# Optimization experiments

Hardware: AMD Instinct MI355X
Metric: run time of the kernel (lower is better)

## Reference

```python
import jax, jax.numpy as jnp
import numpy as np

NUM_HEADS = 8
NUM_LEVEL = 4
KERNEL = 2
NUM_POINT = KERNEL * KERNEL
D_MODEL = 256
HEAD_DIM = D_MODEL // NUM_HEADS
REF_SIZE = 4
EPS = 1e-6


def _kernel_indices():
    # even kernel: linspace(-k/2+0.5, k/2-0.5, k) -> [-0.5, 0.5] for k=2
    ind = np.linspace(-KERNEL // 2 + 0.5, KERNEL // 2 - 0.5, KERNEL)
    i, j = np.meshgrid(ind, ind, indexing='ij')
    ki = np.stack([j, i], axis=-1).reshape(-1, 2) / KERNEL  # (P, 2), (x, y)
    return jnp.asarray(ki, dtype=jnp.float32)


def _ref_windows(shapes):
    # mask is None -> centers on a regular grid, size = ref_size / (H, W)
    refs = []
    for (H, W) in shapes:
        y = (jnp.arange(1, H + 1, dtype=jnp.float32) - 0.5) / (H + EPS)
        x = (jnp.arange(1, W + 1, dtype=jnp.float32) - 0.5) / (W + EPS)
        yy, xx = jnp.meshgrid(y, x, indexing='ij')           # (H, W)
        center = jnp.stack([xx, yy], axis=-1).reshape(-1, 2)  # (HW, 2)
        size = jnp.broadcast_to(
            jnp.array([REF_SIZE / W, REF_SIZE / H], dtype=jnp.float32), center.shape)
        refs.append(jnp.concatenate([center, size], axis=-1))
    return jnp.concatenate(refs, axis=0)  # (L, 4)


def _bilinear_sample(vflat, grid, H, W):
    """vflat: (B, H*W, M, D) one level; grid: (B, Lq, M, P, 2) normalized [0,1].
    Returns (B, Lq, M, P, D). Zero padding outside, align_corners=False."""
    B, _, M, D = vflat.shape
    x = grid[..., 0] * W - 0.5
    y = grid[..., 1] * H - 0.5
    x0 = jnp.floor(x); y0 = jnp.floor(y)
    lx = x - x0; ly = y - y0
    x0i = x0.astype(jnp.int32); y0i = y0.astype(jnp.int32)
    bidx = jnp.arange(B)[:, None, None, None]
    midx = jnp.arange(M)[None, None, :, None]

    def corner(xi, yi, w):
        valid = (xi >= 0) & (xi < W) & (yi >= 0) & (yi < H)
        idx = jnp.clip(yi, 0, H - 1) * W + jnp.clip(xi, 0, W - 1)
        g = vflat[bidx, idx, midx]  # (B, Lq, M, P, D)
        return g * (w * valid.astype(w.dtype))[..., None]

    out = corner(x0i, y0i, (1 - lx) * (1 - ly))
    out = out + corner(x0i + 1, y0i, lx * (1 - ly))
    out = out + corner(x0i, y0i + 1, (1 - lx) * ly)
    out = out + corner(x0i + 1, y0i + 1, lx * ly)
    return out


def setup_inputs() -> dict:
    key = jax.random.key(0)
    ks = jax.random.split(key, 20)
    spatial = [(100, 100), (50, 50), (25, 25), (13, 13)]
    B = 4
    inp = {}
    for i, (H, W) in enumerate(spatial):
        inp[f'value{i}'] = jax.random.normal(ks[i], (B, D_MODEL, H, W), dtype=jnp.float32)
        inp[f'pos{i}'] = jax.random.normal(ks[4 + i], (B, D_MODEL, H, W), dtype=jnp.float32)
    s = 0.05
    inp['Wv'] = jax.random.normal(ks[8], (D_MODEL, D_MODEL), dtype=jnp.float32) * s
    inp['bv'] = jnp.zeros((D_MODEL,), dtype=jnp.float32)
    inp['Wo'] = jax.random.normal(ks[9], (D_MODEL, D_MODEL), dtype=jnp.float32) * s
    inp['bo'] = jnp.zeros((D_MODEL,), dtype=jnp.float32)
    nb = NUM_LEVEL * NUM_HEADS * 4
    inp['Wbox'] = jax.random.normal(ks[10], (nb, D_MODEL), dtype=jnp.float32) * s
    inp['bbox'] = jax.random.uniform(ks[11], (nb,), dtype=jnp.float32)
    na = NUM_HEADS * NUM_LEVEL * NUM_POINT
    inp['Wattn'] = jax.random.normal(ks[12], (na, D_MODEL), dtype=jnp.float32) * s
    inp['battn'] = jax.random.normal(ks[13], (na,), dtype=jnp.float32) * s
    return inp


def reference(value0, value1, value2, value3, pos0, pos1, pos2, pos3,
              Wv, bv, Wo, bo, Wbox, bbox, Wattn, battn):
    levels = [value0, value1, value2, value3]
    poss = [pos0, pos1, pos2, pos3]
    shapes = [(v.shape[2], v.shape[3]) for v in levels]
    B = levels[0].shape[0]

    # flatten pyramid: (B, C, H, W) -> (B, HW, C)
    value = jnp.concatenate(
        [v.reshape(B, D_MODEL, -1).transpose(0, 2, 1) for v in levels], axis=1)
    pos = jnp.concatenate(
        [p.reshape(B, D_MODEL, -1).transpose(0, 2, 1) for p in poss], axis=1)
    L = value.shape[1]

    query = value + pos
    vp = (value @ Wv.T + bv).reshape(B, L, NUM_HEADS, HEAD_DIM)

    attn = jax.nn.softmax(
        (query @ Wattn.T + battn).reshape(B, L, NUM_HEADS, NUM_LEVEL * NUM_POINT),
        axis=-1).reshape(B, L, NUM_HEADS, NUM_LEVEL, NUM_POINT)

    offset = (query @ Wbox.T + bbox).reshape(B, L, NUM_HEADS, NUM_LEVEL, 4)
    ref = _ref_windows(shapes)[None, :, None, None, :]          # (1, L, 1, 1, 4)
    boxes = ref + offset / 8.0 * ref[..., jnp.array([2, 3, 2, 3])]
    center = boxes[..., None, :2]                               # (B, L, M, NL, 1, 2)
    size = boxes[..., None, 2:]
    ki = _kernel_indices()[None, None, None, None, :, :]        # (1,1,1,1,P,2)
    grid = center + ki * jax.nn.relu(size)                      # (B, L, M, NL, P, 2)

    out = jnp.zeros((B, L, NUM_HEADS, HEAD_DIM), dtype=vp.dtype)
    start = 0
    for l, (H, W) in enumerate(shapes):
        end = start + H * W
        vf = vp[:, start:end]                                   # (B, HW, M, D)
        sampled = _bilinear_sample(vf, grid[:, :, :, l], H, W)  # (B, L, M, P, D)
        out = out + jnp.einsum('blmp,blmpd->blmd', attn[:, :, :, l], sampled)
        start = end

    return out.reshape(B, L, D_MODEL) @ Wo.T + bo
```

## Files before the change

### kernel.cpp

```cpp
#include <hip/hip_runtime.h>
#include <cstdint>
#include <cmath>

#define D_MODEL 256
#define NH 8
#define NLVL 4
#define LTOT 13294
#define BATCH 4
#define BTOT (BATCH * LTOT)
#define RPAD 53248

typedef __attribute__((ext_vector_type(8))) short bf8;
typedef __attribute__((ext_vector_type(4))) float f4;
typedef __attribute__((ext_vector_type(2))) float f2;

__device__ __forceinline__ unsigned short f2bf(float x) {
    unsigned u = __float_as_uint(x);
    u += 0x7fffu + ((u >> 16) & 1u);
    return (unsigned short)(u >> 16);
}
__device__ __forceinline__ float bf2f(unsigned short h) {
    return __uint_as_float(((unsigned)h) << 16);
}
__device__ __forceinline__ int swzf(int i, int s) { return s ^ ((i >> 1) & 3); }

__device__ __forceinline__ void level_of(int l, int& lv, int& hw, int& Wl, int& HWl, int& loff) {
    if (l < 10000)      { lv = 0; loff = 0;     Wl = 100; HWl = 10000; }
    else if (l < 12500) { lv = 1; loff = 10000; Wl = 50;  HWl = 2500;  }
    else if (l < 13125) { lv = 2; loff = 12500; Wl = 25;  HWl = 625;   }
    else                { lv = 3; loff = 13125; Wl = 13;  HWl = 169;   }
    hw = l - loff;
}

__global__ __launch_bounds__(256) void pack_weights(
    const float* __restrict__ Wv, const float* __restrict__ Wattn,
    const float* __restrict__ Wbox, const float* __restrict__ Wo,
    unsigned short* __restrict__ W1hi, unsigned short* __restrict__ W1lo,
    unsigned short* __restrict__ Wohi, unsigned short* __restrict__ Wolo) {
    int tid = blockIdx.x * 256 + threadIdx.x;
    const float* src;
    unsigned short *dh, *dl;
    int nb, kb, j, s;
    if (tid < 16384) {
        nb = tid >> 12; kb = (tid >> 9) & 7; j = (tid >> 2) & 127; s = tid & 3;
        int f = nb * 128 + j, c0 = kb * 32 + s * 8;
        if (f < 256)      src = Wv + (size_t)f * 256 + c0;
        else if (f < 384) src = Wattn + (size_t)(f - 256) * 256 + c0;
        else              src = Wbox + (size_t)(f - 384) * 256 + c0;
        dh = W1hi; dl = W1lo;
    } else if (tid < 24576) {
        int t2 = tid - 16384;
        nb = t2 >> 12; kb = (t2 >> 9) & 7; j = (t2 >> 2) & 127; s = t2 & 3;
        int f = nb * 128 + j, c0 = kb * 32 + s * 8;
        src = Wo + (size_t)f * 256 + c0;
        dh = Wohi; dl = Wolo;
    } else return;
    int base = (((nb * 8 + kb) * 128 + j) * 4 + swzf(j, s)) * 8;
    #pragma unroll
    for (int e = 0; e < 8; ++e) {
        float x = src[e];
        unsigned short h = f2bf(x);
        dh[base + e] = h;
        dl[base + e] = f2bf(x - bf2f(h));
    }
}

__global__ __launch_bounds__(256) void convert_A(
    const float* __restrict__ v0, const float* __restrict__ v1,
    const float* __restrict__ v2, const float* __restrict__ v3,
    const float* __restrict__ p0, const float* __restrict__ p1,
    const float* __restrict__ p2, const float* __restrict__ p3,
    unsigned short* __restrict__ Gv, unsigned short* __restrict__ Gq) {
    __shared__ unsigned short HV[64][130];
    __shared__ unsigned short HQ[64][130];
    int t = threadIdx.x;
    int w = t >> 6, lane = t & 63;
    int r0 = blockIdx.x * 64;

    int r = r0 + lane; if (r >= BTOT) r = BTOT - 1;
    int b = r / LTOT, l = r % LTOT;
    int lv, hw, Wl, HWl, loff;
    level_of(l, lv, hw, Wl, HWl, loff);
    const float *vb, *pb;
    switch (lv) { case 0: vb = v0; pb = p0; break; case 1: vb = v1; pb = p1; break;
                  case 2: vb = v2; pb = p2; break; default: vb = v3; pb = p3; break; }
    size_t base = (size_t)b * D_MODEL * (size_t)HWl + (size_t)hw;
    vb += base; pb += base;

    int kb2 = (lane >> 2) & 3, slot = lane & 3;
    for (int h = 0; h < 2; ++h) {
        #pragma unroll 4
        for (int i = 0; i < 32; ++i) {
            int cl = i * 4 + w;
            int c = h * 128 + cl;
            float av = vb[(size_t)c * HWl];
            float aq = av + pb[(size_t)c * HWl];
            HV[lane][cl] = f2bf(av);
            HQ[lane][cl] = f2bf(aq);
        }
        __syncthreads();
        #pragma unroll
        for (int j = 0; j < 8; ++j) {
            int plane = j >> 2;
            int rl = (j & 3) * 16 + w * 4 + (lane >> 4);
            int oct = slot ^ ((rl >> 1) & 3);
            const unsigned* s32 = (const unsigned*)(plane ? &HQ[rl][kb2 * 32 + oct * 8]
                                                          : &HV[rl][kb2 * 32 + oct * 8]);
            uint4 vst = make_uint4(s32[0], s32[1], s32[2], s32[3]);
            unsigned short* dst = (plane ? Gq : Gv)
                + (size_t)(r0 + rl) * 256 + (h * 4 + kb2) * 32 + slot * 8;
            *(uint4*)dst = vst;
        }
        __syncthreads();
    }
}

__global__ __launch_bounds__(256) void gemm1_mfma(
    const unsigned short* __restrict__ Gv, const unsigned short* __restrict__ Gq,
    const unsigned short* __restrict__ W1hi, const unsigned short* __restrict__ W1lo,
    const float* __restrict__ bv, const float* __restrict__ battn, const float* __restrict__ bbox,
    unsigned short* __restrict__ VPb, float* __restrict__ LB) {
    __shared__ __align__(16) unsigned short Ah[2][4096], Bh[2][4096], Bl[2][4096];
    int t = threadIdx.x;
    int nb = blockIdx.x;
    int r0 = blockIdx.y * 128;
    const unsigned short* Asrc = (nb < 2) ? Gv : Gq;
    int w = t >> 6, lane = t & 63;
    int wr = w >> 1, wc = w & 1;
    int row_l = lane & 15, oct = lane >> 4;

    const unsigned short* Bbh = W1hi + (size_t)nb * 32768;
    const unsigned short* Bbl = W1lo + (size_t)nb * 32768;

    f4 acc[4][4];
    #pragma unroll
    for (int i = 0; i < 4; ++i)
        #pragma unroll
        for (int j = 0; j < 4; ++j) acc[i][j] = (f4){0.f, 0.f, 0.f, 0.f};

    int c0 = w * 64 + lane, c1 = c0 + 256;
    const unsigned short* a0b = Asrc + (size_t)(r0 + (c0 >> 2)) * 256 + (c0 & 3) * 8;
    const unsigned short* a1b = Asrc + (size_t)(r0 + (c1 >> 2)) * 256 + (c1 & 3) * 8;

#define G1_STAGE(bb, kb)                                                            \
    {                                                                               \
        __builtin_amdgcn_global_load_lds(a0b + (kb) * 32, &Ah[bb][w * 512], 16, 0, 0);        \
        __builtin_amdgcn_global_load_lds(a1b + (kb) * 32, &Ah[bb][2048 + w * 512], 16, 0, 0); \
        __builtin_amdgcn_global_load_lds(Bbh + (kb) * 4096 + c0 * 8, &Bh[bb][w * 512], 16, 0, 0);        \
        __builtin_amdgcn_global_load_lds(Bbh + (kb) * 4096 + c1 * 8, &Bh[bb][2048 + w * 512], 16, 0, 0); \
        __builtin_amdgcn_global_load_lds(Bbl + (kb) * 4096 + c0 * 8, &Bl[bb][w * 512], 16, 0, 0);        \
        __builtin_amdgcn_global_load_lds(Bbl + (kb) * 4096 + c1 * 8, &Bl[bb][2048 + w * 512], 16, 0, 0); \
    }

    G1_STAGE(0, 0);
    for (int kb = 0; kb < 8; ++kb) {
        __syncthreads();
        if (kb < 7) G1_STAGE((kb + 1) & 1, kb + 1);
        int bb = kb & 1;
        bf8 a[4], bh[4], bl[4];
        #pragma unroll
        for (int x = 0; x < 4; ++x) {
            int ri = wr * 64 + x * 16 + row_l;
            int ci = wc * 64 + x * 16 + row_l;
            a[x]  = *(const bf8*)(&Ah[bb][ri * 32 + swzf(ri, oct) * 8]);
            bh[x] = *(const bf8*)(&Bh[bb][ci * 32 + swzf(ci, oct) * 8]);
            bl[x] = *(const bf8*)(&Bl[bb][ci * 32 + swzf(ci, oct) * 8]);
        }
        #pragma unroll
        for (int mi = 0; mi < 4; ++mi)
            #pragma unroll
            for (int ni = 0; ni < 4; ++ni) {
                f4 c = acc[mi][ni];
                c = __builtin_amdgcn_mfma_f32_16x16x32_bf16(a[mi], bh[ni], c, 0, 0, 0);
                c = __builtin_amdgcn_mfma_f32_16x16x32_bf16(a[mi], bl[ni], c, 0, 0, 0);
                acc[mi][ni] = c;
            }
    }
    #pragma unroll
    for (int ni = 0; ni < 4; ++ni) {
        int col = wc * 64 + ni * 16 + row_l;
        float bias;
        if (nb == 0) bias = bv[col];
        else if (nb == 1) bias = bv[128 + col];
        else if (nb == 2) bias = battn[col];
        else bias = bbox[col];
        #pragma unroll
        for (int mi = 0; mi < 4; ++mi) {
            #pragma unroll
            for (int v = 0; v < 4; ++v) {
                int rr = r0 + wr * 64 + mi * 16 + oct * 4 + v;
                if (rr < BTOT) {
                    float val = acc[mi][ni][v] + bias;
                    if (nb < 2) VPb[(size_t)rr * 256 + nb * 128 + col] = f2bf(val);
                    else        LB[(size_t)rr * 256 + (nb - 2) * 128 + col] = val;
                }
            }
        }
    }
}

__global__ __launch_bounds__(256) void sampler_kernel(const unsigned short* __restrict__ VPb,
                                                      const float* __restrict__ LB,
                                                      unsigned short* __restrict__ att_hi,
                                                      unsigned short* __restrict__ att_lo) {
    __shared__ float sw[16][260];
    const int Ws2[4]   = {100, 50, 25, 13};
    const int offs2[4] = {0, 10000, 12500, 13125};
    int t = threadIdx.x;
    int blk = blockIdx.x;

    {
        int g = t >> 4, p = t & 15;
        int grp = blk * 16 + g;
        int m = grp & 7;
        int r = grp >> 3;
        int l = r % LTOT;
        int rb0 = r - l;

        int lv, hw, Wl, HWl, loff;
        level_of(l, lv, hw, Wl, HWl, loff);
        int x, y;
        switch (lv) {
            case 0:  y = hw / 100; x = hw - y * 100; break;
            case 1:  y = hw / 50;  x = hw - y * 50;  break;
            case 2:  y = hw / 25;  x = hw - y * 25;  break;
            default: y = hw / 13;  x = hw - y * 13;  break;
        }
        float denom = (float)((double)Wl + 1e-6);
        float cx = ((float)x + 0.5f) / denom;
        float cy = ((float)y + 0.5f) / denom;
        float rsw = 4.0f / (float)Wl;

        const float* Lrow = LB + (size_t)r * 256;
        float lg = Lrow[m * 16 + p];
        float mx = lg;
        #pragma unroll
        for (int off = 8; off >= 1; off >>= 1)
            mx = fmaxf(mx, __shfl_xor(mx, off, 16));
        float e = __expf(lg - mx);
        float ssum = e;
        #pragma unroll
        for (int off = 8; off >= 1; off >>= 1)
            ssum += __shfl_xor(ssum, off, 16);
        float aw = e / ssum;

        int lp = p >> 2, pp = p & 3;
        int W2 = Ws2[lp];
        float fW2 = (float)W2;
        float o0 = Lrow[128 + m * 16 + lp * 4 + 0];
        float o1 = Lrow[128 + m * 16 + lp * 4 + 1];
        float o2 = Lrow[128 + m * 16 + lp * 4 + 2];
        float o3 = Lrow[128 + m * 16 + lp * 4 + 3];
        float bcx = cx + o0 * 0.125f * rsw;
        float bcy = cy + o1 * 0.125f * rsw;
        float bsx = fmaxf(fmaf(o2 * 0.125f, rsw, rsw), 0.f);
        float bsy = fmaxf(fmaf(o3 * 0.125f, rsw, rsw), 0.f);
        float kx = (pp & 1)  ? 0.25f : -0.25f;
        float ky = (pp >> 1) ? 0.25f : -0.25f;
        float xs = fmaf(bcx + kx * bsx, fW2, -0.5f);
        float ys = fmaf(bcy + ky * bsy, fW2, -0.5f);
        float x0f = floorf(xs), y0f = floorf(ys);
        float lx = xs - x0f, ly = ys - y0f;
        int x0 = (int)x0f, y0 = (int)y0f;
        int x1 = x0 + 1, y1 = y0 + 1;
        bool vx0 = (x0 >= 0) & (x0 < W2), vx1 = (x1 >= 0) & (x1 < W2);
        bool vy0 = (y0 >= 0) & (y0 < W2), vy1 = (y1 >= 0) & (y1 < W2);
        int x0c = min(max(x0, 0), W2 - 1), x1c = min(max(x1, 0), W2 - 1);
        int y0c = min(max(y0, 0), W2 - 1), y1c = min(max(y1, 0), W2 - 1);
        float w00 = (vx0 & vy0) ? aw * (1.f - lx) * (1.f - ly) : 0.f;
        float w01 = (vx1 & vy0) ? aw * lx * (1.f - ly) : 0.f;
        float w10 = (vx0 & vy1) ? aw * (1.f - lx) * ly : 0.f;
        float w11 = (vx1 & vy1) ? aw * lx * ly : 0.f;
        int rowb = rb0 + offs2[lp];
        int col  = m * 32;
        int i00 = ((rowb + y0c * W2 + x0c) * 256 + col) * 2;
        int i01 = ((rowb + y0c * W2 + x1c) * 256 + col) * 2;
        int i10 = ((rowb + y1c * W2 + x0c) * 256 + col) * 2;
        int i11 = ((rowb + y1c * W2 + x1c) * 256 + col) * 2;
        float* dst = &sw[g][p * 16];
        dst[0] = w00; dst[1] = w00; dst[2] = w01; dst[3] = w01;
        dst[4] = w10; dst[5] = w10; dst[6] = w11; dst[7] = w11;
        dst[8]  = __int_as_float(i00); dst[9]  = __int_as_float(i01);
        dst[10] = __int_as_float(i10); dst[11] = __int_as_float(i11);
    }
    __syncthreads();

    int g = t >> 4, lane16 = t & 15;
    unsigned dby = (unsigned)lane16 * 4u;
    const char* Vb = (const char*)VPb;
    f2 acc2 = {0.f, 0.f};
    #pragma unroll
    for (int p = 0; p < 16; ++p) {
        const float* sp = &sw[g][p * 16];
        float4 wA = *(const float4*)sp;
        float4 wB = *(const float4*)(sp + 4);
        float4 fi = *(const float4*)(sp + 8);
        unsigned u0 = *(const unsigned*)(Vb + (size_t)(__float_as_uint(fi.x) + dby));
        unsigned u1 = *(const unsigned*)(Vb + (size_t)(__float_as_uint(fi.y) + dby));
        unsigned u2 = *(const unsigned*)(Vb + (size_t)(__float_as_uint(fi.z) + dby));
        unsigned u3 = *(const unsigned*)(Vb + (size_t)(__float_as_uint(fi.w) + dby));
        f2 v00 = {__uint_as_float(u0 << 16), __uint_as_float(u0 & 0xffff0000u)};
        f2 v01 = {__uint_as_float(u1 << 16), __uint_as_float(u1 & 0xffff0000u)};
        f2 v10 = {__uint_as_float(u2 << 16), __uint_as_float(u2 & 0xffff0000u)};
        f2 v11 = {__uint_as_float(u3 << 16), __uint_as_float(u3 & 0xffff0000u)};
        acc2 = __builtin_elementwise_fma((f2){wA.x, wA.y}, v00, acc2);
        acc2 = __builtin_elementwise_fma((f2){wA.z, wA.w}, v01, acc2);
        acc2 = __builtin_elementwise_fma((f2){wB.x, wB.y}, v10, acc2);
        acc2 = __builtin_elementwise_fma((f2){wB.z, wB.w}, v11, acc2);
    }
    int grp = blk * 16 + g;
    int m2 = grp & 7, r2 = grp >> 3;
    int d0 = lane16 * 2;
    unsigned short h0 = f2bf(acc2.x), h1 = f2bf(acc2.y);
    unsigned short l0 = f2bf(acc2.x - bf2f(h0)), l1 = f2bf(acc2.y - bf2f(h1));
    size_t base = (size_t)r2 * 256 + m2 * 32 + (((d0 >> 3) ^ ((r2 >> 1) & 3)) << 3) + (d0 & 7);
    *(unsigned*)&att_hi[base] = ((unsigned)h1 << 16) | (unsigned)h0;
    *(unsigned*)&att_lo[base] = ((unsigned)l1 << 16) | (unsigned)l0;
}

__global__ __launch_bounds__(256) void gemm2_mfma(
    const unsigned short* __restrict__ Ahi_g, const unsigned short* __restrict__ Alo_g,
    const unsigned short* __restrict__ Wohi, const unsigned short* __restrict__ Wolo,
    const float* __restrict__ bo, float* __restrict__ out) {
    __shared__ __align__(16) unsigned short Ah[2][4096], Al[2][4096], Bh[2][4096], Bl[2][4096];
    int t = threadIdx.x;
    int nb = blockIdx.x;
    int r0 = blockIdx.y * 128;
    int w = t >> 6, lane = t & 63;
    int wr = w >> 1, wc = w & 1;
    int row_l = lane & 15, oct = lane >> 4;

    const unsigned short* Bbh = Wohi + (size_t)nb * 32768;
    const unsigned short* Bbl = Wolo + (size_t)nb * 32768;

    f4 acc[4][4];
    #pragma unroll
    for (int i = 0; i < 4; ++i)
        #pragma unroll
        for (int j = 0; j < 4; ++j) acc[i][j] = (f4){0.f, 0.f, 0.f, 0.f};

    int c0 = w * 64 + lane, c1 = c0 + 256;
    int ra0 = r0 + (c0 >> 2); if (ra0 >= BTOT) ra0 = BTOT - 1;
    int ra1 = r0 + (c1 >> 2); if (ra1 >= BTOT) ra1 = BTOT - 1;
    const unsigned short* ah0 = Ahi_g + (size_t)ra0 * 256 + (c0 & 3) * 8;
    const unsigned short* ah1 = Ahi_g + (size_t)ra1 * 256 + (c1 & 3) * 8;
    const unsigned short* al0 = Alo_g + (size_t)ra0 * 256 + (c0 & 3) * 8;
    const unsigned short* al1 = Alo_g + (size_t)ra1 * 256 + (c1 & 3) * 8;

#define G2_STAGE(bb, kb)                                                            \
    {                                                                               \
        __builtin_amdgcn_global_load_lds(ah0 + (kb) * 32, &Ah[bb][w * 512], 16, 0, 0);        \
        __builtin_amdgcn_global_load_lds(ah1 + (kb) * 32, &Ah[bb][2048 + w * 512], 16, 0, 0); \
        __builtin_amdgcn_global_load_lds(al0 + (kb) * 32, &Al[bb][w * 512], 16, 0, 0);        \
        __builtin_amdgcn_global_load_lds(al1 + (kb) * 32, &Al[bb][2048 + w * 512], 16, 0, 0); \
        __builtin_amdgcn_global_load_lds(Bbh + (kb) * 4096 + c0 * 8, &Bh[bb][w * 512], 16, 0, 0);        \
        __builtin_amdgcn_global_load_lds(Bbh + (kb) * 4096 + c1 * 8, &Bh[bb][2048 + w * 512], 16, 0, 0); \
        __builtin_amdgcn_global_load_lds(Bbl + (kb) * 4096 + c0 * 8, &Bl[bb][w * 512], 16, 0, 0);        \
        __builtin_amdgcn_global_load_lds(Bbl + (kb) * 4096 + c1 * 8, &Bl[bb][2048 + w * 512], 16, 0, 0); \
    }

    G2_STAGE(0, 0);
    for (int kb = 0; kb < 8; ++kb) {
        __syncthreads();
        if (kb < 7) G2_STAGE((kb + 1) & 1, kb + 1);
        int bb = kb & 1;
        bf8 ah[4], al[4], bh[4], bl[4];
        #pragma unroll
        for (int x = 0; x < 4; ++x) {
            int ri = wr * 64 + x * 16 + row_l;
            int ci = wc * 64 + x * 16 + row_l;
            ah[x] = *(const bf8*)(&Ah[bb][ri * 32 + swzf(ri, oct) * 8]);
            al[x] = *(const bf8*)(&Al[bb][ri * 32 + swzf(ri, oct) * 8]);
            bh[x] = *(const bf8*)(&Bh[bb][ci * 32 + swzf(ci, oct) * 8]);
            bl[x] = *(const bf8*)(&Bl[bb][ci * 32 + swzf(ci, oct) * 8]);
        }
        #pragma unroll
        for (int mi = 0; mi < 4; ++mi)
            #pragma unroll
            for (int ni = 0; ni < 4; ++ni) {
                f4 c = acc[mi][ni];
                c = __builtin_amdgcn_mfma_f32_16x16x32_bf16(ah[mi], bh[ni], c, 0, 0, 0);
                c = __builtin_amdgcn_mfma_f32_16x16x32_bf16(ah[mi], bl[ni], c, 0, 0, 0);
                c = __builtin_amdgcn_mfma_f32_16x16x32_bf16(al[mi], bh[ni], c, 0, 0, 0);
                acc[mi][ni] = c;
            }
    }
    #pragma unroll
    for (int ni = 0; ni < 4; ++ni) {
        int col = wc * 64 + ni * 16 + row_l;
        float bias = bo[nb * 128 + col];
        #pragma unroll
        for (int mi = 0; mi < 4; ++mi) {
            #pragma unroll
            for (int v = 0; v < 4; ++v) {
                int rr = r0 + wr * 64 + mi * 16 + oct * 4 + v;
                if (rr < BTOT)
                    out[(size_t)rr * 256 + nb * 128 + col] = acc[mi][ni][v] + bias;
            }
        }
    }
}

extern "C" void kernel_launch(void* const* d_in, const int* in_sizes, int n_in,
                              void* d_out, int out_size, void* d_ws, size_t ws_size,
                              hipStream_t stream) {
    const float* v0 = (const float*)d_in[0];
    const float* p0 = (const float*)d_in[1];
    const float* v1 = (const float*)d_in[2];
    const float* p1 = (const float*)d_in[3];
    const float* v2 = (const float*)d_in[4];
    const float* p2 = (const float*)d_in[5];
    const float* v3 = (const float*)d_in[6];
    const float* p3 = (const float*)d_in[7];
    const float* Wv    = (const float*)d_in[8];
    const float* bv    = (const float*)d_in[9];
    const float* Wo    = (const float*)d_in[10];
    const float* bo    = (const float*)d_in[11];
    const float* Wbox  = (const float*)d_in[12];
    const float* bbox  = (const float*)d_in[13];
    const float* Wattn = (const float*)d_in[14];
    const float* battn = (const float*)d_in[15];
    float* out = (float*)d_out;

    char* ws = (char*)d_ws;
    unsigned short* W1hi = (unsigned short*)(ws);
    unsigned short* W1lo = (unsigned short*)(ws + 262144);
    unsigned short* Wohi = (unsigned short*)(ws + 524288);
    unsigned short* Wolo = (unsigned short*)(ws + 655360);
    unsigned short* Gv   = (unsigned short*)(ws + 1048576);
    unsigned short* Gq   = (unsigned short*)(ws + 1048576 + 27262976);
    unsigned short* atth = Gv;
    unsigned short* attl = Gq;
    unsigned short* VPb  = (unsigned short*)(ws + 1048576 + 2 * 27262976);
    float*          LB   = (float*)(ws + 1048576 + 2 * 27262976 + 27226112);

    convert_A<<<dim3(RPAD / 64), dim3(256), 0, stream>>>(v0, v1, v2, v3,
                                                         p0, p1, p2, p3, Gv, Gq);
    pack_weights<<<dim3(96), dim3(256), 0, stream>>>(Wv, Wattn, Wbox, Wo,
                                                     W1hi, W1lo, Wohi, Wolo);

    gemm1_mfma<<<dim3(4, RPAD / 128), dim3(256), 0, stream>>>(
        Gv, Gq, W1hi, W1lo, bv, battn, bbox, VPb, LB);

    sampler_kernel<<<dim3((BTOT * NH) / 16), dim3(256), 0, stream>>>(VPb, LB, atth, attl);

    gemm2_mfma<<<dim3(2, (BTOT + 127) / 128), dim3(256), 0, stream>>>(
        atth, attl, Wohi, Wolo, bo, out);
}
```

Measured before the change: 245.5 us.

## Widen sampler gathers to 16-byte loads with 4 lanes per head group

The sampler kernel now assigns 4 threads per (row, head) group instead of 16, so each thread gathers 8 bf16 channels with uint4 loads rather than 2 channels with 32-bit loads. Each block handles 64 groups, with the setup phase run in 4 passes and shared-memory entries compacted to 8 floats (weights no longer duplicated). Outputs are written as 16-byte vector stores with the same swizzle. This cuts the number of gather instructions and shared-memory traffic, at the cost of fewer threads in flight per byte and more registers per thread.

```diff
diff --git a/kernel.cpp b/kernel.cpp
--- a/kernel.cpp
+++ b/kernel.cpp
@@ -21,6 +21,9 @@
 }
 __device__ __forceinline__ float bf2f(unsigned short h) {
     return __uint_as_float(((unsigned)h) << 16);
+}
+__device__ __forceinline__ f2 up2(unsigned u) {
+    return (f2){__uint_as_float(u << 16), __uint_as_float(u & 0xffff0000u)};
 }
 __device__ __forceinline__ int swzf(int i, int s) { return s ^ ((i >> 1) & 3); }
 
@@ -203,15 +206,17 @@
                                                       const float* __restrict__ LB,
                                                       unsigned short* __restrict__ att_hi,
                                                       unsigned short* __restrict__ att_lo) {
-    __shared__ float sw[16][260];
+    __shared__ float sw[64][132];
     const int Ws2[4]   = {100, 50, 25, 13};
     const int offs2[4] = {0, 10000, 12500, 13125};
     int t = threadIdx.x;
     int blk = blockIdx.x;
 
-    {
-        int g = t >> 4, p = t & 15;
-        int grp = blk * 16 + g;
+    #pragma unroll
+    for (int pass = 0; pass < 4; ++pass) {
+        int g = (t >> 4) + pass * 16;
+        int p = t & 15;
+        int grp = blk * 64 + g;
         int m = grp & 7;
         int r = grp >> 3;
         int l = r % LTOT;
@@ -277,45 +282,59 @@
         int i01 = ((rowb + y0c * W2 + x1c) * 256 + col) * 2;
         int i10 = ((rowb + y1c * W2 + x0c) * 256 + col) * 2;
         int i11 = ((rowb + y1c * W2 + x1c) * 256 + col) * 2;
-        float* dst = &sw[g][p * 16];
-        dst[0] = w00; dst[1] = w00; dst[2] = w01; dst[3] = w01;
-        dst[4] = w10; dst[5] = w10; dst[6] = w11; dst[7] = w11;
-        dst[8]  = __int_as_float(i00); dst[9]  = __int_as_float(i01);
-        dst[10] = __int_as_float(i10); dst[11] = __int_as_float(i11);
+        float* dst = &sw[g][p * 8];
+        *(float4*)dst       = (float4){w00, w01, w10, w11};
+        *(float4*)(dst + 4) = (float4){__int_as_float(i00), __int_as_float(i01),
+                                       __int_as_float(i10), __int_as_float(i11)};
     }
     __syncthreads();
 
-    int g = t >> 4, lane16 = t & 15;
-    unsigned dby = (unsigned)lane16 * 4u;
+    int g = t >> 2, lane4 = t & 3;
+    unsigned dby = (unsigned)lane4 * 16u;
     const char* Vb = (const char*)VPb;
-    f2 acc2 = {0.f, 0.f};
+    f2 a01 = {0.f, 0.f}, a23 = {0.f, 0.f}, a45 = {0.f, 0.f}, a67 = {0.f, 0.f};
     #pragma unroll
     for (int p = 0; p < 16; ++p) {
-        const float* sp = &sw[g][p * 16];
-        float4 wA = *(const float4*)sp;
-        float4 wB = *(const float4*)(sp + 4);
-        float4 fi = *(const float4*)(sp + 8);
-        unsigned u0 = *(const unsigned*)(Vb + (size_t)(__float_as_uint(fi.x) + dby));
-        unsigned u1 = *(const unsigned*)(Vb + (size_t)(__float_as_uint(fi.y) + dby));
-        unsigned u2 = *(const unsigned*)(Vb + (size_t)(__float_as_uint(fi.z) + dby));
-        unsigned u3 = *(const unsigned*)(Vb + (size_t)(__float_as_uint(fi.w) + dby));
-        f2 v00 = {__uint_as_float(u0 << 16), __uint_as_float(u0 & 0xffff0000u)};
-        f2 v01 = {__uint_as_float(u1 << 16), __uint_as_float(u1 & 0xffff0000u)};
-        f2 v10 = {__uint_as_float(u2 << 16), __uint_as_float(u2 & 0xffff0000u)};
-        f2 v11 = {__uint_as_float(u3 << 16), __uint_as_float(u3 & 0xffff0000u)};
-        acc2 = __builtin_elementwise_fma((f2){wA.x, wA.y}, v00, acc2);
-        acc2 = __builtin_elementwise_fma((f2){wA.z, wA.w}, v01, acc2);
-        acc2 = __builtin_elementwise_fma((f2){wB.x, wB.y}, v10, acc2);
-        acc2 = __builtin_elementwise_fma((f2){wB.z, wB.w}, v11, acc2);
-    }
-    int grp = blk * 16 + g;
+        const float* sp = &sw[g][p * 8];
+        float4 wv = *(const float4*)sp;
+        float4 fi = *(const float4*)(sp + 4);
+        uint4 u00 = *(const uint4*)(Vb + (size_t)(__float_as_uint(fi.x) + dby));
+        uint4 u01 = *(const uint4*)(Vb + (size_t)(__float_as_uint(fi.y) + dby));
+        uint4 u10 = *(const uint4*)(Vb + (size_t)(__float_as_uint(fi.z) + dby));
+        uint4 u11 = *(const uint4*)(Vb + (size_t)(__float_as_uint(fi.w) + dby));
+        f2 w0 = {wv.x, wv.x}, w1 = {wv.y, wv.y}, w2 = {wv.z, wv.z}, w3 = {wv.w, wv.w};
+        a01 = __builtin_elementwise_fma(w0, up2(u00.x), a01);
+        a23 = __builtin_elementwise_fma(w0, up2(u00.y), a23);
+        a45 = __builtin_elementwise_fma(w0, up2(u00.z), a45);
+        a67 = __builtin_elementwise_fma(w0, up2(u00.w), a67);
+        a01 = __builtin_elementwise_fma(w1, up2(u01.x), a01);
+        a23 = __builtin_elementwise_fma(w1, up2(u01.y), a23);
+        a45 = __builtin_elementwise_fma(w1, up2(u01.z), a45);
+        a67 = __builtin_elementwise_fma(w1, up2(u01.w), a67);
+        a01 = __builtin_elementwise_fma(w2, up2(u10.x), a01);
+        a23 = __builtin_elementwise_fma(w2, up2(u10.y), a23);
+        a45 = __builtin_elementwise_fma(w2, up2(u10.z), a45);
+        a67 = __builtin_elementwise_fma(w2, up2(u10.w), a67);
+        a01 = __builtin_elementwise_fma(w3, up2(u11.x), a01);
+        a23 = __builtin_elementwise_fma(w3, up2(u11.y), a23);
+        a45 = __builtin_elementwise_fma(w3, up2(u11.z), a45);
+        a67 = __builtin_elementwise_fma(w3, up2(u11.w), a67);
+    }
+    int grp = blk * 64 + g;
     int m2 = grp & 7, r2 = grp >> 3;
-    int d0 = lane16 * 2;
-    unsigned short h0 = f2bf(acc2.x), h1 = f2bf(acc2.y);
-    unsigned short l0 = f2bf(acc2.x - bf2f(h0)), l1 = f2bf(acc2.y - bf2f(h1));
-    size_t base = (size_t)r2 * 256 + m2 * 32 + (((d0 >> 3) ^ ((r2 >> 1) & 3)) << 3) + (d0 & 7);
-    *(unsigned*)&att_hi[base] = ((unsigned)h1 << 16) | (unsigned)h0;
-    *(unsigned*)&att_lo[base] = ((unsigned)l1 << 16) | (unsigned)l0;
+    int slot = lane4 ^ ((r2 >> 1) & 3);
+    size_t base = (size_t)r2 * 256 + m2 * 32 + slot * 8;
+    float av[8] = {a01.x, a01.y, a23.x, a23.y, a45.x, a45.y, a67.x, a67.y};
+    unsigned hp[4], lp4[4];
+    #pragma unroll
+    for (int q = 0; q < 4; ++q) {
+        unsigned short h0 = f2bf(av[q * 2]), h1 = f2bf(av[q * 2 + 1]);
+        unsigned short l0 = f2bf(av[q * 2] - bf2f(h0)), l1 = f2bf(av[q * 2 + 1] - bf2f(h1));
+        hp[q]  = ((unsigned)h1 << 16) | h0;
+        lp4[q] = ((unsigned)l1 << 16) | l0;
+    }
+    *(uint4*)&att_hi[base] = make_uint4(hp[0], hp[1], hp[2], hp[3]);
+    *(uint4*)&att_lo[base] = make_uint4(lp4[0], lp4[1], lp4[2], lp4[3]);
 }
 
 __global__ __launch_bounds__(256) void gemm2_mfma(
@@ -442,7 +461,7 @@
     gemm1_mfma<<<dim3(4, RPAD / 128), dim3(256), 0, stream>>>(
         Gv, Gq, W1hi, W1lo, bv, battn, bbox, VPb, LB);
 
-    sampler_kernel<<<dim3((BTOT * NH) / 16), dim3(256), 0, stream>>>(VPb, LB, atth, attl);
+    sampler_kernel<<<dim3((BTOT * NH) / 64), dim3(256), 0, stream>>>(VPb, LB, atth, attl);
 
     gemm2_mfma<<<dim3(2, (BTOT + 127) / 128), dim3(256), 0, stream>>>(
         atth, attl, Wohi, Wolo, bo, out);
```

New measurement: 237.4 us. -3.3%, faster.
